# Kernel tuning notes

Hardware: AMD Instinct MI355X
Metric: run time of the kernel (lower is better)

The kernel has to match this reference:

```python
import jax, jax.numpy as jnp
import numpy as np
import math

S, D, H, HD = 2048, 1280, 16, 80  # seq_len, embed_dim, num_heads, head_dim


def setup_inputs() -> dict:
    key = jax.random.key(0)
    k1, k2, k3, k4, k5, k6 = jax.random.split(key, 6)
    hidden_states = jax.random.normal(k1, (S, D), dtype=jnp.float32)
    # 4 equal-length segments (e.g. 4 images of 512 patches)
    cu_seqlens = jnp.array([0, 512, 1024, 1536, 2048], dtype=jnp.int32)
    # RoPE theta*position angles, [S, HD//2]
    rotary_pos_emb = jax.random.uniform(k2, (S, HD // 2), dtype=jnp.float32) * 10.0
    qkv_w = jax.random.normal(k3, (3 * D, D), dtype=jnp.float32) * 0.02
    qkv_b = jax.random.normal(k4, (3 * D,), dtype=jnp.float32) * 0.02
    proj_w = jax.random.normal(k5, (D, D), dtype=jnp.float32) * 0.02
    proj_b = jax.random.normal(k6, (D,), dtype=jnp.float32) * 0.02
    return {"hidden_states": hidden_states, "cu_seqlens": cu_seqlens,
            "rotary_pos_emb": rotary_pos_emb, "qkv_w": qkv_w, "qkv_b": qkv_b,
            "proj_w": proj_w, "proj_b": proj_b}


def _rotate_half(x):
    x1, x2 = jnp.split(x, 2, axis=-1)
    return jnp.concatenate([-x2, x1], axis=-1)


def _square_mask(n, seq, dtype):
    # faithful translation of rewrite_loop_for_square_mask on a full-min mask
    neg = jnp.finfo(dtype).min
    mask = jnp.full((1, n, n), neg, dtype=dtype)
    r = jnp.arange(n)
    less0 = (r[:, None] < seq[None, :]).astype(jnp.int32)
    less = less0.sum(axis=-1, keepdims=True) + 1            # [n,1] segment label
    sq = less * less.T                                       # [n,n]
    c1 = jnp.logical_or(seq.min() == 0, less != less.max())
    c2 = jnp.logical_or(seq.max() == n, less != less.min())
    look = (c1 & c2).astype(jnp.int32) * less
    filt = (sq != look ** 2).astype(dtype)                   # 0 inside blocks, 1 outside
    return mask * filt


def reference(hidden_states, cu_seqlens, rotary_pos_emb, qkv_w, qkv_b, proj_w, proj_b):
    seq_len = hidden_states.shape[0]
    qkv = hidden_states @ qkv_w.T + qkv_b                    # [S, 3D]
    qkv = qkv.reshape(seq_len, 3, H, HD)
    q, k, v = qkv[:, 0], qkv[:, 1], qkv[:, 2]                # [S, H, HD]

    # rotary_pos_emb path: emb = cat(rope, rope), cos/sin broadcast over heads
    emb = jnp.concatenate([rotary_pos_emb, rotary_pos_emb], axis=-1)  # [S, HD]
    cos = jnp.cos(emb)[:, None, :]                           # [S, 1, HD]
    sin = jnp.sin(emb)[:, None, :]
    q = q * cos + _rotate_half(q) * sin
    k = k * cos + _rotate_half(k) * sin

    mask = _square_mask(seq_len, cu_seqlens, q.dtype)        # [1, S, S]

    qh = q.transpose(1, 0, 2)                                # [H, S, HD]
    kh = k.transpose(1, 0, 2)
    vh = v.transpose(1, 0, 2)

    attn = jnp.einsum('hqd,hkd->hqk', qh, kh) / math.sqrt(HD)  # [H, S, S]
    attn = attn + mask
    attn = jax.nn.softmax(attn.astype(jnp.float32), axis=-1).astype(q.dtype)
    out = jnp.einsum('hqk,hkd->hqd', attn, vh)               # [H, S, HD]
    out = out.transpose(1, 0, 2).reshape(seq_len, -1)        # [S, D]
    return out @ proj_w.T + proj_b
```

## Files before the change

kernel.cpp:

```cpp
#include <hip/hip_runtime.h>


typedef unsigned short u16;
typedef short short8 __attribute__((ext_vector_type(8)));
typedef float floatx4 __attribute__((ext_vector_type(4)));
typedef u16 ushort4v __attribute__((ext_vector_type(4)));
typedef float float4v __attribute__((ext_vector_type(4)));
typedef float float2v __attribute__((ext_vector_type(2)));

#define S_LEN 2048
#define DMODEL 1280
#define NHEAD 16
#define HDIM 80
#define HDIM_P 96
#define SEGS 4
#define SEG_LEN 512
#define QSCALE 0.11180339887498948f

__device__ __forceinline__ float b2f(u16 u) {
  union { unsigned int i; float f; } v; v.i = ((unsigned int)u) << 16; return v.f;
}
__device__ __forceinline__ u16 f2b(float f) {
  union { float f; unsigned int i; } v; v.f = f;
  unsigned int i = v.i;
  return (u16)((i + 0x7FFFu + ((i >> 16) & 1u)) >> 16);
}

__device__ __forceinline__ void load_lds16(const u16* g, u16* l) {
  __builtin_amdgcn_global_load_lds(
      (const __attribute__((address_space(1))) unsigned int*)g,
      (__attribute__((address_space(3))) unsigned int*)l, 16, 0, 0);
}

__device__ __forceinline__ unsigned int rope_perm(unsigned int j) {
  if (j >= 2560u) return j;
  unsigned int sec = j / 1280u;
  unsigned int jj = j - sec * 1280u;
  unsigned int h = jj / 80u, d = jj - h * 80u;
  unsigned int dp = (d < 40u) ? (2u * d) : (2u * (d - 40u) + 1u);
  return sec * 1280u + h * 80u + dp;
}

__global__ __launch_bounds__(256) void convert_all(
    const void* __restrict__ s_hid, const void* __restrict__ s_qw,
    const void* __restrict__ s_pw,  const void* __restrict__ s_rope,
    const void* __restrict__ s_qb,  const void* __restrict__ s_pb,
    u16* __restrict__ d_hid, u16* __restrict__ d_qw, u16* __restrict__ d_pw,
    u16* __restrict__ d_qb, u16* __restrict__ d_pb,
    int* __restrict__ flag_out, float* __restrict__ cs_tab,
    float* __restrict__ sn_tab) {
  unsigned int w = ((const unsigned int*)s_rope)[threadIdx.x & 63];
  int is_f32 = __any((int)((w >> 15) & 1));
  if (blockIdx.x == 0 && threadIdx.x == 0) *flag_out = is_f32;

  unsigned int qi = blockIdx.x * 256 + threadIdx.x;

  if (qi >= 2295040u) {
    unsigned int ti = qi - 2295040u;
    float ang = is_f32 ? ((const float*)s_rope)[ti]
                       : b2f(((const u16*)s_rope)[ti]);
    cs_tab[ti] = cosf(ang);
    sn_tab[ti] = sinf(ang);
    return;
  }

  if (qi >= 2293760u && qi < 2294720u) {
    unsigned int off = qi - 2293760u;
    ushort4v o;
    if (is_f32) {
      float4v f = ((const float4v*)s_qb)[off];
      #pragma unroll
      for (int i = 0; i < 4; ++i) o[i] = f2b(f[i]);
    } else {
      o = ((const ushort4v*)s_qb)[off];
    }
    #pragma unroll
    for (int e = 0; e < 4; ++e) d_qb[rope_perm(off * 4u + e)] = o[e];
    return;
  }

  const void* src; u16* dst; unsigned int off, doff;
  if      (qi < 655360u)  { src = s_hid;  dst = d_hid;  off = qi;            doff = off; }
  else if (qi < 1884160u) {
    src = s_qw; dst = d_qw; off = qi - 655360u;
    unsigned int row = off / 320u, col = off - row * 320u;
    doff = rope_perm(row) * 320u + col;
  }
  else if (qi < 2293760u) { src = s_pw;   dst = d_pw;   off = qi - 1884160u; doff = off; }
  else                    { src = s_pb;   dst = d_pb;   off = qi - 2294720u; doff = off; }
  ushort4v o;
  if (is_f32) {
    float4v f = ((const float4v*)src)[off];
    #pragma unroll
    for (int i = 0; i < 4; ++i) o[i] = f2b(f[i]);
  } else {
    o = ((const ushort4v*)src)[off];
  }
  ((ushort4v*)dst)[doff] = o;
}

__global__ __launch_bounds__(256) void gemm_qkv(
    const u16* __restrict__ A, const u16* __restrict__ W,
    const u16* __restrict__ bias,
    u16* __restrict__ qh, u16* __restrict__ kh, u16* __restrict__ vt,
    const float* __restrict__ cs, const float* __restrict__ sn) {
  const int K = DMODEL;
  __shared__ __attribute__((aligned(16))) u16 As[2][128 * 64];
  __shared__ __attribute__((aligned(16))) u16 Bs[2][128 * 64];
  int wave = threadIdx.x >> 6, lane = threadIdx.x & 63;
  int r = lane & 15, q = lane >> 4;
  int wm = wave >> 1, wn = wave & 1;

  int id = blockIdx.x + 30 * blockIdx.y;
  int xcd = id & 7, slot = id >> 3;
  int bx = slot % 30;
  int by = 2 * xcd + slot / 30;
  int m0 = by * 128, n0 = bx * 128;
  const int isV = (n0 >= 2 * DMODEL);

  int srow = lane >> 3;
  int sg   = (lane & 7) ^ srow;
  const u16* Ab = A + (size_t)(m0 + srow) * K + sg * 8;
  const u16* Wb = W + (size_t)(n0 + srow) * K + sg * 8;

  floatx4 acc[4][4];
  #pragma unroll
  for (int a = 0; a < 4; ++a)
    #pragma unroll
    for (int b = 0; b < 4; ++b) acc[a][b] = (floatx4){0.f, 0.f, 0.f, 0.f};

  #pragma unroll
  for (int c = 0; c < 4; ++c) {
    int ch = wave * 4 + c;
    load_lds16(Ab + (size_t)(ch * 8) * K, &As[0][ch * 8 * 64]);
    load_lds16(Wb + (size_t)(ch * 8) * K, &Bs[0][ch * 8 * 64]);
  }
  int buf = 0;
  for (int kt = 0; kt < K; kt += 64, buf ^= 1) {
    __syncthreads();
    if (kt + 64 < K) {
      #pragma unroll
      for (int c = 0; c < 4; ++c) {
        int ch = wave * 4 + c;
        load_lds16(Ab + kt + 64 + (size_t)(ch * 8) * K, &As[buf ^ 1][ch * 8 * 64]);
        load_lds16(Wb + kt + 64 + (size_t)(ch * 8) * K, &Bs[buf ^ 1][ch * 8 * 64]);
      }
    }
    #pragma unroll
    for (int ks = 0; ks < 2; ++ks) {
      short8 af[4], bf[4];
      #pragma unroll
      for (int i = 0; i < 4; ++i) {
        int arow = wm * 64 + i * 16 + r;
        int brow = wn * 64 + i * 16 + r;
        af[i] = *(const short8*)&As[buf][arow * 64 + (((ks * 4 + q) ^ (arow & 7)) * 8)];
        bf[i] = *(const short8*)&Bs[buf][brow * 64 + (((ks * 4 + q) ^ (brow & 7)) * 8)];
      }
      if (isV) {
        #pragma unroll
        for (int mi = 0; mi < 4; ++mi)
          #pragma unroll
          for (int ni = 0; ni < 4; ++ni)
            acc[mi][ni] = __builtin_amdgcn_mfma_f32_16x16x32_bf16(af[mi], bf[ni],
                                                                  acc[mi][ni], 0, 0, 0);
      } else {
        #pragma unroll
        for (int ni = 0; ni < 4; ++ni)
          #pragma unroll
          for (int mi = 0; mi < 4; ++mi)
            acc[ni][mi] = __builtin_amdgcn_mfma_f32_16x16x32_bf16(bf[ni], af[mi],
                                                                  acc[ni][mi], 0, 0, 0);
      }
    }
  }

  if (!isV) {
    #pragma unroll
    for (int ni = 0; ni < 4; ++ni) {
      int fbase = n0 + wn * 64 + ni * 16 + q * 4;
      int isq = fbase < DMODEL;
      int c2 = fbase - (isq ? 0 : DMODEL);
      int h = c2 / HDIM, cin = c2 - h * HDIM;
      float scale = isq ? QSCALE : 1.0f;
      u16* dstb = (isq ? qh : kh) + (size_t)h * S_LEN * HDIM_P + cin;
      ushort4v bv4 = *(const ushort4v*)&bias[fbase];
      float b0 = b2f(bv4[0]), b1 = b2f(bv4[1]);
      float b2v = b2f(bv4[2]), b3 = b2f(bv4[3]);
      int idx0 = cin >> 1;
      #pragma unroll
      for (int mi = 0; mi < 4; ++mi) {
        int s = m0 + wm * 64 + mi * 16 + r;
        float2v c2v = *(const float2v*)(cs + (size_t)s * 40 + idx0);
        float2v s2v = *(const float2v*)(sn + (size_t)s * 40 + idx0);
        float a0 = acc[ni][mi][0] + b0;
        float a1 = acc[ni][mi][1] + b1;
        float a2 = acc[ni][mi][2] + b2v;
        float a3 = acc[ni][mi][3] + b3;
        ushort4v o;
        o[0] = f2b((a0 * c2v[0] - a1 * s2v[0]) * scale);
        o[1] = f2b((a1 * c2v[0] + a0 * s2v[0]) * scale);
        o[2] = f2b((a2 * c2v[1] - a3 * s2v[1]) * scale);
        o[3] = f2b((a3 * c2v[1] + a2 * s2v[1]) * scale);
        *(ushort4v*)(dstb + (size_t)s * HDIM_P) = o;
      }
    }
  } else {
    #pragma unroll
    for (int ni = 0; ni < 4; ++ni) {
      int col = n0 + wn * 64 + ni * 16 + r;
      float bv = b2f(bias[col]);
      int c2 = col - 2 * DMODEL;
      #pragma unroll
      for (int mi = 0; mi < 4; ++mi) {
        int row0 = m0 + wm * 64 + mi * 16 + q * 4;
        ushort4v pk;
        #pragma unroll
        for (int i = 0; i < 4; ++i) pk[i] = f2b(acc[mi][ni][i] + bv);
        *(ushort4v*)(vt + (size_t)c2 * S_LEN + row0) = pk;
      }
    }
  }
}

#define PPAD 136
#define OPAD 84
struct WaveScratch {
  union {
    u16   P[32][PPAD];
    float O[32][OPAD];
  };
};
__global__ __launch_bounds__(256) void flash_attn(
    const u16* __restrict__ qh, const u16* __restrict__ kh,
    const u16* __restrict__ vt, const int* __restrict__ cu,
    u16* __restrict__ attn_out) {
  __shared__ __attribute__((aligned(16))) WaveScratch wsc[4];
  int wave = threadIdx.x >> 6, lane = threadIdx.x & 63;
  int r = lane & 15, q = lane >> 4;
  int hz = blockIdx.x;
  int seg = hz & (SEGS - 1), h = hz >> 2;
  int base = cu[seg];
  int m0 = blockIdx.y * 64;
  int k0 = wave * 128;

  const short8 zero8 = {0, 0, 0, 0, 0, 0, 0, 0};
  const u16* Qb = qh + ((size_t)h * S_LEN + base + m0 + r) * HDIM_P + q * 8;
  short8 aq[4][3];
  #pragma unroll
  for (int t = 0; t < 4; ++t) {
    const u16* Qt = Qb + (size_t)(t * 16) * HDIM_P;
    aq[t][0] = *(const short8*)(Qt);
    aq[t][1] = *(const short8*)(Qt + 32);
    aq[t][2] = (q < 2) ? *(const short8*)(Qt + 64) : zero8;
  }

  const u16* Kb = kh + ((size_t)h * S_LEN + base + k0 + r) * HDIM_P + q * 8;
  const u16* Vb = vt + ((size_t)h * HDIM + r) * S_LEN + base + k0 + q * 8;

  ushort4v stash[2][8];
  #pragma unroll
  for (int g = 0; g < 8; ++g) {
    const u16* Kg = Kb + (size_t)(16 * g) * HDIM_P;
    short8 kf0 = *(const short8*)(Kg);
    short8 kf1 = *(const short8*)(Kg + 32);
    short8 kf2 = (q < 2) ? *(const short8*)(Kg + 64) : zero8;
    #pragma unroll
    for (int t = 0; t < 4; ++t) {
      floatx4 s = {0.f, 0.f, 0.f, 0.f};
      s = __builtin_amdgcn_mfma_f32_16x16x32_bf16(kf0, aq[t][0], s, 0, 0, 0);
      s = __builtin_amdgcn_mfma_f32_16x16x32_bf16(kf1, aq[t][1], s, 0, 0, 0);
      s = __builtin_amdgcn_mfma_f32_16x16x32_bf16(kf2, aq[t][2], s, 0, 0, 0);
      ushort4v pw;
      #pragma unroll
      for (int i = 0; i < 4; ++i) pw[i] = f2b(__expf(s[i]));
      if (t < 2)
        *(ushort4v*)&wsc[wave].P[t * 16 + r][g * 16 + q * 4] = pw;
      else
        stash[t - 2][g] = pw;
    }
  }

  const short8 ones = {0x3F80, 0x3F80, 0x3F80, 0x3F80, 0x3F80, 0x3F80, 0x3F80, 0x3F80};
  #pragma unroll
  for (int half = 0; half < 2; ++half) {
    if (half == 1) {
      __syncthreads();
      #pragma unroll
      for (int t = 0; t < 2; ++t)
        #pragma unroll
        for (int g = 0; g < 8; ++g)
          *(ushort4v*)&wsc[wave].P[t * 16 + r][g * 16 + q * 4] = stash[t][g];
    }
    floatx4 o[2][5], o5[2];
    #pragma unroll
    for (int t = 0; t < 2; ++t) {
      o5[t] = (floatx4){0.f, 0.f, 0.f, 0.f};
      #pragma unroll
      for (int t5 = 0; t5 < 5; ++t5) o[t][t5] = (floatx4){0.f, 0.f, 0.f, 0.f};
    }
    #pragma unroll
    for (int kq = 0; kq < 4; ++kq) {
      short8 pa0 = *(const short8*)&wsc[wave].P[r][kq * 32 + q * 8];
      short8 pa1 = *(const short8*)&wsc[wave].P[16 + r][kq * 32 + q * 8];
      #pragma unroll
      for (int t5 = 0; t5 < 5; ++t5) {
        short8 bv = *(const short8*)(Vb + kq * 32 + (size_t)(t5 * 16) * S_LEN);
        o[0][t5] = __builtin_amdgcn_mfma_f32_16x16x32_bf16(bv, pa0, o[0][t5], 0, 0, 0);
        o[1][t5] = __builtin_amdgcn_mfma_f32_16x16x32_bf16(bv, pa1, o[1][t5], 0, 0, 0);
      }
      o5[0] = __builtin_amdgcn_mfma_f32_16x16x32_bf16(ones, pa0, o5[0], 0, 0, 0);
      o5[1] = __builtin_amdgcn_mfma_f32_16x16x32_bf16(ones, pa1, o5[1], 0, 0, 0);
    }
    #pragma unroll
    for (int t = 0; t < 2; ++t)
      #pragma unroll
      for (int t5 = 0; t5 < 5; ++t5)
        *(float4v*)&wsc[wave].O[t * 16 + r][t5 * 16 + q * 4] = o[t][t5];
    if (q == 0) {
      wsc[wave].O[r][80]      = o5[0][0];
      wsc[wave].O[16 + r][80] = o5[1][0];
    }
    __syncthreads();

    int tid = threadIdx.x;
    int row = tid >> 3;
    int c0 = (tid & 7) * 10;
    float L = wsc[0].O[row][80] + wsc[1].O[row][80] +
              wsc[2].O[row][80] + wsc[3].O[row][80];
    float invL = 1.0f / L;
    u16* Or = attn_out +
        (size_t)(base + m0 + half * 32 + row) * DMODEL + h * HDIM + c0;
    #pragma unroll
    for (int j = 0; j < 10; ++j) {
      float v = wsc[0].O[row][c0 + j] + wsc[1].O[row][c0 + j] +
                wsc[2].O[row][c0 + j] + wsc[3].O[row][c0 + j];
      Or[j] = f2b(v * invL);
    }
  }
}

__global__ __launch_bounds__(256) void gemm_tiled(
    const u16* __restrict__ A, const u16* __restrict__ W,
    const u16* __restrict__ bias, void* __restrict__ C,
    int M, int N, int K, const int* __restrict__ out_flag) {
  __shared__ __attribute__((aligned(16))) u16 As[2][64 * 64];
  __shared__ __attribute__((aligned(16))) u16 Bs[2][128 * 64];
  int wave = threadIdx.x >> 6, lane = threadIdx.x & 63;
  int r = lane & 15, q = lane >> 4;
  int wm = wave >> 1, wn = wave & 1;

  int bx = blockIdx.x, by = blockIdx.y;
  if (gridDim.x == 10 && gridDim.y == 32) {
    int id = bx + 10 * by;
    int xcd = id & 7, slot = id >> 3;
    bx = slot % 10;
    by = 4 * xcd + slot / 10;
  }
  int m0 = by * 64, n0 = bx * 128;

  int srow = lane >> 3;
  int sg   = (lane & 7) ^ srow;
  const u16* Ab = A + (size_t)(m0 + srow) * K + sg * 8;
  const u16* Wb = W + (size_t)(n0 + srow) * K + sg * 8;

  floatx4 acc[2][4];
  #pragma unroll
  for (int mi = 0; mi < 2; ++mi)
    #pragma unroll
    for (int ni = 0; ni < 4; ++ni) acc[mi][ni] = (floatx4){0.f, 0.f, 0.f, 0.f};

  #pragma unroll
  for (int c = 0; c < 2; ++c)
    load_lds16(Ab + (size_t)((wave * 2 + c) * 8) * K, &As[0][(wave * 2 + c) * 8 * 64]);
  #pragma unroll
  for (int c = 0; c < 4; ++c)
    load_lds16(Wb + (size_t)((wave * 4 + c) * 8) * K, &Bs[0][(wave * 4 + c) * 8 * 64]);

  int buf = 0;
  for (int kt = 0; kt < K; kt += 64, buf ^= 1) {
    __syncthreads();
    if (kt + 64 < K) {
      #pragma unroll
      for (int c = 0; c < 2; ++c)
        load_lds16(Ab + kt + 64 + (size_t)((wave * 2 + c) * 8) * K,
                   &As[buf ^ 1][(wave * 2 + c) * 8 * 64]);
      #pragma unroll
      for (int c = 0; c < 4; ++c)
        load_lds16(Wb + kt + 64 + (size_t)((wave * 4 + c) * 8) * K,
                   &Bs[buf ^ 1][(wave * 4 + c) * 8 * 64]);
    }
    #pragma unroll
    for (int ks = 0; ks < 2; ++ks) {
      short8 af[2], bf[4];
      #pragma unroll
      for (int i = 0; i < 2; ++i) {
        int arow = wm * 32 + i * 16 + r;
        af[i] = *(const short8*)&As[buf][arow * 64 + (((ks * 4 + q) ^ (arow & 7)) * 8)];
      }
      #pragma unroll
      for (int i = 0; i < 4; ++i) {
        int brow = wn * 64 + i * 16 + r;
        bf[i] = *(const short8*)&Bs[buf][brow * 64 + (((ks * 4 + q) ^ (brow & 7)) * 8)];
      }
      #pragma unroll
      for (int mi = 0; mi < 2; ++mi)
        #pragma unroll
        for (int ni = 0; ni < 4; ++ni)
          acc[mi][ni] = __builtin_amdgcn_mfma_f32_16x16x32_bf16(af[mi], bf[ni],
                                                                acc[mi][ni], 0, 0, 0);
    }
  }

  int f32out = out_flag ? *out_flag : 0;
  #pragma unroll
  for (int ni = 0; ni < 4; ++ni) {
    int col = n0 + wn * 64 + ni * 16 + r;
    float bv = b2f(bias[col]);
    #pragma unroll
    for (int mi = 0; mi < 2; ++mi) {
      size_t row0 = (size_t)(m0 + wm * 32 + mi * 16 + q * 4);
      if (f32out) {
        float* out = (float*)C;
        #pragma unroll
        for (int i = 0; i < 4; ++i) out[(row0 + i) * N + col] = acc[mi][ni][i] + bv;
      } else {
        u16* out = (u16*)C;
        #pragma unroll
        for (int i = 0; i < 4; ++i) out[(row0 + i) * N + col] = f2b(acc[mi][ni][i] + bv);
      }
    }
  }
}

extern "C" void kernel_launch(void* const* d_in, const int* in_sizes, int n_in,
                              void* d_out, int out_size, void* d_ws, size_t ws_size,
                              hipStream_t stream) {
  const void* hidden_r = d_in[0];
  const int*  cu       = (const int*)d_in[1];
  const void* rope_r   = d_in[2];
  const void* qkv_w_r  = d_in[3];
  const void* qkv_b_r  = d_in[4];
  const void* proj_w_r = d_in[5];
  const void* proj_b_r = d_in[6];

  char* ws = (char*)d_ws;
  u16* hidden_c = (u16*)(ws);
  u16* qkvw_c   = (u16*)(ws +  6291456u);
  u16* projw_c  = (u16*)(ws + 16777216u);
  u16* qkvb_c   = (u16*)(ws + 21135360u);
  u16* projb_c  = (u16*)(ws + 21143040u);
  int* flag     = (int*)(ws + 21145600u);
  float* cs_tab = (float*)(ws + 22020096u);
  float* sn_tab = (float*)(ws + 22347776u);
  u16* qh       = (u16*)(ws + 25165824u);
  u16* kh       = (u16*)(ws + 31457280u);
  u16* vt       = (u16*)(ws + 37748736u);
  u16* attn_out = (u16*)(ws + 44040192u);

  convert_all<<<dim3(9285), dim3(256), 0, stream>>>(
      hidden_r, qkv_w_r, proj_w_r, rope_r, qkv_b_r, proj_b_r,
      hidden_c, qkvw_c, projw_c, qkvb_c, projb_c, flag, cs_tab, sn_tab);

  gemm_qkv<<<dim3(3840 / 128, 2048 / 128), dim3(256), 0, stream>>>(
      hidden_c, qkvw_c, qkvb_c, qh, kh, vt, cs_tab, sn_tab);

  flash_attn<<<dim3(NHEAD * SEGS, SEG_LEN / 64), dim3(256), 0, stream>>>(
      qh, kh, vt, cu, attn_out);

  gemm_tiled<<<dim3(1280 / 128, 2048 / 64), dim3(256), 0, stream>>>(
      attn_out, projw_c, projb_c, d_out, S_LEN, DMODEL, DMODEL, flag);
}
```

Baseline: 162.3 us.

## Fold log2e into Q scale, use exp2 and native bf16 conversion, reorder rope table

Folds log2(e) into the Q scaling so the attention softmax can use the hardware exp2 instruction directly instead of __expf. Replaces the hand-written round-to-nearest-even bf16 conversion with the HIP __float2bfloat16 intrinsic, which may lower to a native conversion instruction on this target. Moves the rope cos/sin table computation to the first blocks of the conversion kernel, shifting the other offsets. The goal is fewer ALU instructions in the attention inner loop and in the epilogues, while rounding behaviour should stay equivalent.

After: 159.4 us (median of 2 runs). About the same (-1.7%).

```diff
diff --git a/kernel.cpp b/kernel.cpp
--- a/kernel.cpp
+++ b/kernel.cpp
@@ -1,4 +1,5 @@
 #include <hip/hip_runtime.h>
+#include <hip/hip_bf16.h>
 
 
 typedef unsigned short u16;
@@ -16,6 +17,7 @@
 #define SEGS 4
 #define SEG_LEN 512
 #define QSCALE 0.11180339887498948f
+#define QSCALE2 (0.11180339887498948f * 1.4426950408889634f)
 
 __device__ __forceinline__ float b2f(u16 u) {
   union { unsigned int i; float f; } v; v.i = ((unsigned int)u) << 16; return v.f;
@@ -24,6 +26,10 @@
   union { float f; unsigned int i; } v; v.f = f;
   unsigned int i = v.i;
   return (u16)((i + 0x7FFFu + ((i >> 16) & 1u)) >> 16);
+}
+__device__ __forceinline__ u16 f2bh(float f) {
+  __hip_bfloat16 h = __float2bfloat16(f);
+  union { __hip_bfloat16 h; u16 u; } v; v.h = h; return v.u;
 }
 
 __device__ __forceinline__ void load_lds16(const u16* g, u16* l) {
@@ -55,17 +61,16 @@
 
   unsigned int qi = blockIdx.x * 256 + threadIdx.x;
 
-  if (qi >= 2295040u) {
-    unsigned int ti = qi - 2295040u;
-    float ang = is_f32 ? ((const float*)s_rope)[ti]
-                       : b2f(((const u16*)s_rope)[ti]);
-    cs_tab[ti] = cosf(ang);
-    sn_tab[ti] = sinf(ang);
+  if (qi < 81920u) {
+    float ang = is_f32 ? ((const float*)s_rope)[qi]
+                       : b2f(((const u16*)s_rope)[qi]);
+    cs_tab[qi] = cosf(ang);
+    sn_tab[qi] = sinf(ang);
     return;
   }
 
-  if (qi >= 2293760u && qi < 2294720u) {
-    unsigned int off = qi - 2293760u;
+  if (qi >= 2375680u && qi < 2376640u) {
+    unsigned int off = qi - 2375680u;
     ushort4v o;
     if (is_f32) {
       float4v f = ((const float4v*)s_qb)[off];
@@ -80,14 +85,14 @@
   }
 
   const void* src; u16* dst; unsigned int off, doff;
-  if      (qi < 655360u)  { src = s_hid;  dst = d_hid;  off = qi;            doff = off; }
-  else if (qi < 1884160u) {
-    src = s_qw; dst = d_qw; off = qi - 655360u;
+  if      (qi < 737280u)  { src = s_hid;  dst = d_hid;  off = qi - 81920u;   doff = off; }
+  else if (qi < 1966080u) {
+    src = s_qw; dst = d_qw; off = qi - 737280u;
     unsigned int row = off / 320u, col = off - row * 320u;
     doff = rope_perm(row) * 320u + col;
   }
-  else if (qi < 2293760u) { src = s_pw;   dst = d_pw;   off = qi - 1884160u; doff = off; }
-  else                    { src = s_pb;   dst = d_pb;   off = qi - 2294720u; doff = off; }
+  else if (qi < 2375680u) { src = s_pw;   dst = d_pw;   off = qi - 1966080u; doff = off; }
+  else                    { src = s_pb;   dst = d_pb;   off = qi - 2376640u; doff = off; }
   ushort4v o;
   if (is_f32) {
     float4v f = ((const float4v*)src)[off];
@@ -181,7 +186,7 @@
       int isq = fbase < DMODEL;
       int c2 = fbase - (isq ? 0 : DMODEL);
       int h = c2 / HDIM, cin = c2 - h * HDIM;
-      float scale = isq ? QSCALE : 1.0f;
+      float scale = isq ? QSCALE2 : 1.0f;
       u16* dstb = (isq ? qh : kh) + (size_t)h * S_LEN * HDIM_P + cin;
       ushort4v bv4 = *(const ushort4v*)&bias[fbase];
       float b0 = b2f(bv4[0]), b1 = b2f(bv4[1]);
@@ -197,10 +202,10 @@
         float a2 = acc[ni][mi][2] + b2v;
         float a3 = acc[ni][mi][3] + b3;
         ushort4v o;
-        o[0] = f2b((a0 * c2v[0] - a1 * s2v[0]) * scale);
-        o[1] = f2b((a1 * c2v[0] + a0 * s2v[0]) * scale);
-        o[2] = f2b((a2 * c2v[1] - a3 * s2v[1]) * scale);
-        o[3] = f2b((a3 * c2v[1] + a2 * s2v[1]) * scale);
+        o[0] = f2bh((a0 * c2v[0] - a1 * s2v[0]) * scale);
+        o[1] = f2bh((a1 * c2v[0] + a0 * s2v[0]) * scale);
+        o[2] = f2bh((a2 * c2v[1] - a3 * s2v[1]) * scale);
+        o[3] = f2bh((a3 * c2v[1] + a2 * s2v[1]) * scale);
         *(ushort4v*)(dstb + (size_t)s * HDIM_P) = o;
       }
     }
@@ -215,7 +220,7 @@
         int row0 = m0 + wm * 64 + mi * 16 + q * 4;
         ushort4v pk;
         #pragma unroll
-        for (int i = 0; i < 4; ++i) pk[i] = f2b(acc[mi][ni][i] + bv);
+        for (int i = 0; i < 4; ++i) pk[i] = f2bh(acc[mi][ni][i] + bv);
         *(ushort4v*)(vt + (size_t)c2 * S_LEN + row0) = pk;
       }
     }
@@ -272,7 +277,7 @@
       s = __builtin_amdgcn_mfma_f32_16x16x32_bf16(kf2, aq[t][2], s, 0, 0, 0);
       ushort4v pw;
       #pragma unroll
-      for (int i = 0; i < 4; ++i) pw[i] = f2b(__expf(s[i]));
+      for (int i = 0; i < 4; ++i) pw[i] = f2bh(__builtin_amdgcn_exp2f(s[i]));
       if (t < 2)
         *(ushort4v*)&wsc[wave].P[t * 16 + r][g * 16 + q * 4] = pw;
       else
@@ -334,7 +339,7 @@
     for (int j = 0; j < 10; ++j) {
       float v = wsc[0].O[row][c0 + j] + wsc[1].O[row][c0 + j] +
                 wsc[2].O[row][c0 + j] + wsc[3].O[row][c0 + j];
-      Or[j] = f2b(v * invL);
+      Or[j] = f2bh(v * invL);
     }
   }
 }
@@ -426,7 +431,7 @@
       } else {
         u16* out = (u16*)C;
         #pragma unroll
-        for (int i = 0; i < 4; ++i) out[(row0 + i) * N + col] = f2b(acc[mi][ni][i] + bv);
+        for (int i = 0; i < 4; ++i) out[(row0 + i) * N + col] = f2bh(acc[mi][ni][i] + bv);
       }
     }
   }
```
